# Performance work log

Measured on AMD Instinct MI355X. Metric: run time of the kernel, lower is better.

Reference implementation:

```python
import jax, jax.numpy as jnp
import numpy as np

EMB, HEADS, T_BLK = 1024, 16, 2048
B, T = 2, 2048
HD = EMB // HEADS


def setup_inputs() -> dict:
    key = jax.random.key(0)
    ks = jax.random.split(key, 9)
    s = 1.0 / np.sqrt(EMB)
    return {
        "x": jax.random.normal(ks[0], (B, T, EMB), jnp.float32),
        "Wq": jax.random.normal(ks[1], (EMB, EMB), jnp.float32) * s,
        "bq": jax.random.normal(ks[2], (EMB,), jnp.float32) * s,
        "Wk": jax.random.normal(ks[3], (EMB, EMB), jnp.float32) * s,
        "bk": jax.random.normal(ks[4], (EMB,), jnp.float32) * s,
        "Wv": jax.random.normal(ks[5], (EMB, EMB), jnp.float32) * s,
        "bv": jax.random.normal(ks[6], (EMB,), jnp.float32) * s,
        "Wo": jax.random.normal(ks[7], (EMB, EMB), jnp.float32) * s,
        "bo": jax.random.normal(ks[8], (EMB,), jnp.float32) * s,
    }


def reference(x, Wq, bq, Wk, bk, Wv, bv, Wo, bo):
    # eval mode: dropout is identity
    Bn, Tn, C = x.shape
    def proj(W, b):
        y = x @ W.T + b                      # [B,T,C]
        return y.reshape(Bn, Tn, HEADS, HD).transpose(0, 2, 1, 3)  # [B,H,T,hd]
    q, k, v = proj(Wq, bq), proj(Wk, bk), proj(Wv, bv)
    scores = jnp.einsum('bhqd,bhkd->bhqk', q, k) * (HD ** -0.5)  # [B,H,T,T]
    causal = jnp.tril(jnp.ones((Tn, Tn), dtype=bool))
    scores = jnp.where(causal, scores, -jnp.inf)
    w = jax.nn.softmax(scores, axis=-1)
    out = jnp.einsum('bhqk,bhkd->bhqd', w, v)                    # [B,H,T,hd]
    out = out.transpose(0, 2, 1, 3).reshape(Bn, Tn, C)
    return out @ Wo.T + bo
```

## Files before the change

### kernel.cpp

```cpp
#include <hip/hip_runtime.h>
#include <stdint.h>

#define EMB   1024
#define HEADS 16
#define HD    64
#define BB    2
#define TT    2048
#define MTOT  (BB*TT)
#define LDA   72
#define LDP   72

#define ELX (4194304u)
#define ELW (1048576u)

#define CSCALE (0.125f * 1.44269504088896f)

typedef __attribute__((ext_vector_type(8))) short short8;
typedef __attribute__((ext_vector_type(4))) float f32x4;
typedef __attribute__((ext_vector_type(4))) unsigned short us4;

__device__ __forceinline__ float bf2f(ushort u) {
  union { uint32_t u; float f; } x; x.u = ((uint32_t)u) << 16; return x.f;
}
__device__ __forceinline__ ushort f2bf(float f) {
  union { float f; uint32_t u; } x; x.f = f;
  uint32_t u = x.u;
  u += 0x7fffu + ((u >> 16) & 1u);
  return (ushort)(u >> 16);
}
__device__ __forceinline__ ushort f2bf_trunc(float f) {
  union { float f; uint32_t u; } x; x.f = f;
  return (ushort)(x.u >> 16);
}
__device__ __forceinline__ uint32_t pack2(uint32_t lo, uint32_t hi) {
  return (lo >> 16) | (hi & 0xFFFF0000u);
}
__device__ __forceinline__ short8 pack8(f32x4 a, f32x4 b) {
  union { f32x4 v; uint32_t u[4]; } A, B;
  A.v = a; B.v = b;
  union { uint32_t d[4]; short8 s; } R;
  R.d[0] = pack2(A.u[0], A.u[1]);
  R.d[1] = pack2(A.u[2], A.u[3]);
  R.d[2] = pack2(B.u[0], B.u[1]);
  R.d[3] = pack2(B.u[2], B.u[3]);
  return R.s;
}
__device__ __forceinline__ short8 cvt8_rne(const float* f) {
  f32x4 a = *(const f32x4*)f;
  f32x4 b = *(const f32x4*)(f + 4);
  short8 r;
  r[0] = (short)f2bf(a[0]); r[1] = (short)f2bf(a[1]);
  r[2] = (short)f2bf(a[2]); r[3] = (short)f2bf(a[3]);
  r[4] = (short)f2bf(b[0]); r[5] = (short)f2bf(b[1]);
  r[6] = (short)f2bf(b[2]); r[7] = (short)f2bf(b[3]);
  return r;
}

__global__ void detect_dtype(const uint32_t* __restrict__ x, int* __restrict__ flag) {
  const int lane = threadIdx.x & 63;
  int cnt = 0;
#pragma unroll
  for (int i = 0; i < 4; ++i) {
    const uint32_t v = x[lane * 4 + i];
    const uint32_t e = ((v & 0xFFFFu) >> 7) & 0xFFu;
    cnt += (e >= 0x70u && e <= 0x8Fu) ? 1 : 0;
  }
#pragma unroll
  for (int off = 1; off < 64; off <<= 1) cnt += __shfl_xor(cnt, off);
  if (lane == 0) *flag = (cnt > 128) ? 1 : 0;
}

__global__ __launch_bounds__(256) void convert3(const void* __restrict__ w0,
                                                const void* __restrict__ w1,
                                                const void* __restrict__ w2,
                                                ushort* __restrict__ dst,
                                                const int* __restrict__ flag) {
  const size_t i = ((size_t)blockIdx.x * 256 + threadIdx.x) * 8;
  const int wi = (int)(i >> 20);
  const size_t off = i & (ELW - 1);
  const void* src = (wi == 0) ? w0 : (wi == 1) ? w1 : w2;
  if (*flag) *(short8*)(dst + i) = *(const short8*)((const ushort*)src + off);
  else       *(short8*)(dst + i) = cvt8_rne((const float*)src + off);
}

template<bool ABF>
__device__ __forceinline__ void gemm_qkv64(const void* __restrict__ Ap,
                                           const ushort* __restrict__ Wp,
                                           int m0, int n0,
                                           ushort* As, ushort* Ws,
                                           f32x4 acc[4][2]) {
  const int tid  = threadIdx.x;
  const int w    = tid >> 6;
  const int lane = tid & 63;
  const int quad = lane >> 4;
  const int l16  = lane & 15;
  const int arow = tid >> 2;
  const int acol = (tid & 3) * 16;
  const int brow = tid >> 1;
  const int bcol = (tid & 1) * 32;

  const size_t aoff = (size_t)(m0 + arow) * EMB + acol;
  const size_t boff = (size_t)(n0 + brow) * EMB + bcol;

  short8 ab[3][2];
  f32x4  af[3][4];
  short8 wb[3][4];

#pragma unroll
  for (int s = 0; s < 2; ++s) {
    if constexpr (ABF) {
      ab[s][0] = *(const short8*)((const ushort*)Ap + aoff + 64 * s);
      ab[s][1] = *(const short8*)((const ushort*)Ap + aoff + 64 * s + 8);
    } else {
#pragma unroll
      for (int i = 0; i < 4; ++i)
        af[s][i] = *(const f32x4*)((const float*)Ap + aoff + 64 * s + 4 * i);
    }
#pragma unroll
    for (int i = 0; i < 4; ++i)
      wb[s][i] = *(const short8*)(Wp + boff + 64 * s + 8 * i);
  }

#pragma unroll
  for (int it = 0; it < 16; ++it) {
    const int k0 = it * 64;
    const int cur = it % 3, nxt = (it + 2) % 3;
    __syncthreads();
    if constexpr (ABF) {
      *(short8*)&As[arow * LDP + acol]     = ab[cur][0];
      *(short8*)&As[arow * LDP + acol + 8] = ab[cur][1];
    } else {
      *(short8*)&As[arow * LDP + acol]     = pack8(af[cur][0], af[cur][1]);
      *(short8*)&As[arow * LDP + acol + 8] = pack8(af[cur][2], af[cur][3]);
    }
#pragma unroll
    for (int i = 0; i < 4; ++i) *(short8*)&Ws[brow * LDP + bcol + 8 * i] = wb[cur][i];
    if (it + 2 < 16) {
      const int kn = k0 + 128;
      if constexpr (ABF) {
        ab[nxt][0] = *(const short8*)((const ushort*)Ap + aoff + kn);
        ab[nxt][1] = *(const short8*)((const ushort*)Ap + aoff + kn + 8);
      } else {
#pragma unroll
        for (int i = 0; i < 4; ++i)
          af[nxt][i] = *(const f32x4*)((const float*)Ap + aoff + kn + 4 * i);
      }
#pragma unroll
      for (int i = 0; i < 4; ++i)
        wb[nxt][i] = *(const short8*)(Wp + boff + kn + 8 * i);
    }
    __syncthreads();

#pragma unroll
    for (int ks = 0; ks < 2; ++ks) {
      short8 a_[4], b_[2];
#pragma unroll
      for (int i = 0; i < 4; ++i)
        a_[i] = *(const short8*)&As[(i * 16 + l16) * LDP + ks * 32 + quad * 8];
#pragma unroll
      for (int i = 0; i < 2; ++i)
        b_[i] = *(const short8*)&Ws[(w * 32 + i * 16 + l16) * LDP + ks * 32 + quad * 8];
#pragma unroll
      for (int mi = 0; mi < 4; ++mi)
#pragma unroll
        for (int ni = 0; ni < 2; ++ni)
          acc[mi][ni] = __builtin_amdgcn_mfma_f32_16x16x32_bf16(a_[mi], b_[ni], acc[mi][ni], 0, 0, 0);
    }
  }
}

__device__ __forceinline__ void qkv_epi64(f32x4 acc[4][2], int mt, int n0, int mat,
                                          const void* bias, int isbf,
                                          ushort* qo, ushort* ko, ushort* vo) {
  const int tid  = threadIdx.x;
  const int w    = tid >> 6;
  const int lane = tid & 63;
  const int quad = lane >> 4;
  const int l16  = lane & 15;
  ushort* dst = (mat == 0) ? qo : ko;
  const float sc = (mat == 0) ? CSCALE : 1.0f;

#pragma unroll
  for (int ni = 0; ni < 2; ++ni) {
    const int n = n0 + w * 32 + ni * 16 + l16;
    const float bv_ = isbf ? bf2f(((const ushort*)bias)[n]) : ((const float*)bias)[n];
    const int hh = n >> 6, d = n & 63;
#pragma unroll
    for (int mi = 0; mi < 4; ++mi) {
      const int mbase = mt * 64 + mi * 16 + quad * 4;
      const int b = mbase >> 11, t = mbase & (TT - 1);
      if (mat == 2) {
        us4 pk;
#pragma unroll
        for (int r = 0; r < 4; ++r) pk[r] = f2bf(acc[mi][ni][r] + bv_);
        *(us4*)&vo[((size_t)((b * HEADS + hh) * HD + d)) * TT + t] = pk;
      } else {
#pragma unroll
        for (int r = 0; r < 4; ++r)
          dst[((size_t)((b * HEADS + hh) * TT + t + r)) * HD + d] = f2bf((acc[mi][ni][r] + bv_) * sc);
      }
    }
  }
}

__global__ __launch_bounds__(256) void qkv_pipe(const void* __restrict__ x,
                                                const ushort* __restrict__ w3,
                                                const void* __restrict__ bq,
                                                const void* __restrict__ bk,
                                                const void* __restrict__ bv,
                                                ushort* __restrict__ qo,
                                                ushort* __restrict__ ko,
                                                ushort* __restrict__ vo,
                                                const int* __restrict__ flag) {
  __shared__ __align__(16) ushort As[64 * LDP];
  __shared__ __align__(16) ushort Ws[128 * LDP];
  const int xcd = blockIdx.x & 7;
  const int i   = blockIdx.x >> 3;
  const int nt  = xcd * 3 + (i % 3);
  const int mt  = i / 3;
  const int mat = nt >> 3;
  const int n0  = (nt & 7) * 128;
  const ushort* W  = w3 + (size_t)mat * ELW;
  const void* bias = (mat == 0) ? bq : (mat == 1) ? bk : bv;

  f32x4 acc[4][2];
#pragma unroll
  for (int a = 0; a < 4; ++a)
#pragma unroll
    for (int b = 0; b < 2; ++b) acc[a][b] = (f32x4){0.f, 0.f, 0.f, 0.f};

  const int isbf = *flag;
  if (isbf) gemm_qkv64<true >(x, W, mt * 64, n0, As, Ws, acc);
  else      gemm_qkv64<false>(x, W, mt * 64, n0, As, Ws, acc);
  qkv_epi64(acc, mt, n0, mat, bias, isbf, qo, ko, vo);
}

__global__ __launch_bounds__(256) void attn3(const ushort* __restrict__ qw,
                                             const ushort* __restrict__ kw,
                                             const ushort* __restrict__ vtw,
                                             ushort* __restrict__ out) {
  __shared__ __align__(16) ushort Ks[64 * LDA];
  __shared__ __align__(16) ushort Vts[64 * LDA];
  __shared__ __align__(16) ushort Ps[4][16 * LDA];

  const int bid = blockIdx.x;
  const int j  = bid >> 8;
  const int r8 = bid & 255;
  const int qh = r8 & 31;
  const int bh = j * 8 + (r8 >> 5);
  int qt;
  if      (j == 0) qt = qh;
  else if (j == 1) qt = 31 - qh;
  else if (j == 2) qt = (qh + 16) & 31;
  else             qt = 31 - ((qh + 16) & 31);
  const int h = bh & (HEADS - 1);
  const int b = bh >> 4;

  const int tid  = threadIdx.x;
  const int w    = tid >> 6;
  const int lane = tid & 63;
  const int quad = lane >> 4;
  const int l16  = lane & 15;

  const size_t hoff = ((size_t)(b * HEADS + h)) * TT * HD;
  const ushort* Qg = qw + hoff;
  const ushort* Kg = kw + hoff;
  const ushort* Vg = vtw + hoff;
  const int q0 = qt * 64;

  short8 qf[2];
  {
    const ushort* qrow = Qg + (size_t)(q0 + w * 16 + l16) * HD;
    qf[0] = *(const short8*)(qrow + quad * 8);
    qf[1] = *(const short8*)(qrow + 32 + quad * 8);
  }

  const int row = tid >> 2;
  const int c0  = (tid & 3) * 16;
  const ushort* Kbase = Kg + (size_t)row * HD + c0;
  const ushort* Vbase = Vg + (size_t)row * TT + c0;

  float ls[4] = {0.f, 0.f, 0.f, 0.f};
  f32x4 O[4];
#pragma unroll
  for (int ni = 0; ni < 4; ++ni) O[ni] = (f32x4){0.f, 0.f, 0.f, 0.f};

  auto compute_tile = [&](int kt) {
    f32x4 s[4];
#pragma unroll
    for (int ni = 0; ni < 4; ++ni) s[ni] = (f32x4){0.f, 0.f, 0.f, 0.f};
#pragma unroll
    for (int ks = 0; ks < 2; ++ks) {
#pragma unroll
      for (int ni = 0; ni < 4; ++ni) {
        short8 kb = *(const short8*)&Ks[(ni * 16 + l16) * LDA + ks * 32 + quad * 8];
        s[ni] = __builtin_amdgcn_mfma_f32_16x16x32_bf16(qf[ks], kb, s[ni], 0, 0, 0);
      }
    }
    if (kt == qt) {
#pragma unroll
      for (int ni = 0; ni < 4; ++ni) {
        const int kk = ni * 16 + l16;
#pragma unroll
        for (int r = 0; r < 4; ++r)
          if (kk > w * 16 + quad * 4 + r) s[ni][r] = -__builtin_inff();
      }
    }
#pragma unroll
    for (int ni = 0; ni < 4; ++ni)
#pragma unroll
      for (int r = 0; r < 4; ++r) {
        const float p = exp2f(s[ni][r]);
        s[ni][r] = p;
        ls[r] += p;
      }
#pragma unroll
    for (int ni = 0; ni < 4; ++ni)
#pragma unroll
      for (int r = 0; r < 4; ++r)
        Ps[w][(quad * 4 + r) * LDA + ni * 16 + l16] = f2bf_trunc(s[ni][r]);
#pragma unroll
    for (int ks = 0; ks < 2; ++ks) {
      short8 a = *(const short8*)&Ps[w][l16 * LDA + ks * 32 + quad * 8];
#pragma unroll
      for (int ni = 0; ni < 4; ++ni) {
        short8 vb = *(const short8*)&Vts[(ni * 16 + l16) * LDA + ks * 32 + quad * 8];
        O[ni] = __builtin_amdgcn_mfma_f32_16x16x32_bf16(a, vb, O[ni], 0, 0, 0);
      }
    }
  };

  short8 ak0, ak1, av0, av1;
  short8 bk0, bk1, bv0, bv1;

  ak0 = *(const short8*)(Kbase);
  ak1 = *(const short8*)(Kbase + 8);
  av0 = *(const short8*)(Vbase);
  av1 = *(const short8*)(Vbase + 8);

  for (int kt = 0; kt <= qt; ) {
    __syncthreads();
    *(short8*)&Ks[row * LDA + c0]      = ak0;
    *(short8*)&Ks[row * LDA + c0 + 8]  = ak1;
    *(short8*)&Vts[row * LDA + c0]     = av0;
    *(short8*)&Vts[row * LDA + c0 + 8] = av1;
    if (kt + 1 <= qt) {
      const size_t ko_ = (size_t)(kt + 1) * 64 * HD;
      bk0 = *(const short8*)(Kbase + ko_);
      bk1 = *(const short8*)(Kbase + ko_ + 8);
      bv0 = *(const short8*)(Vbase + (kt + 1) * 64);
      bv1 = *(const short8*)(Vbase + (kt + 1) * 64 + 8);
    }
    __syncthreads();
    compute_tile(kt);
    ++kt;
    if (kt > qt) break;

    __syncthreads();
    *(short8*)&Ks[row * LDA + c0]      = bk0;
    *(short8*)&Ks[row * LDA + c0 + 8]  = bk1;
    *(short8*)&Vts[row * LDA + c0]     = bv0;
    *(short8*)&Vts[row * LDA + c0 + 8] = bv1;
    if (kt + 1 <= qt) {
      const size_t ko_ = (size_t)(kt + 1) * 64 * HD;
      ak0 = *(const short8*)(Kbase + ko_);
      ak1 = *(const short8*)(Kbase + ko_ + 8);
      av0 = *(const short8*)(Vbase + (kt + 1) * 64);
      av1 = *(const short8*)(Vbase + (kt + 1) * 64 + 8);
    }
    __syncthreads();
    compute_tile(kt);
    ++kt;
  }

#pragma unroll
  for (int r = 0; r < 4; ++r) {
#pragma unroll
    for (int off = 1; off < 16; off <<= 1) ls[r] += __shfl_xor(ls[r], off);
    const float inv = 1.0f / ls[r];
    const int t = q0 + w * 16 + quad * 4 + r;
#pragma unroll
    for (int ni = 0; ni < 4; ++ni) {
      out[((size_t)(b * TT + t)) * EMB + h * HD + ni * 16 + l16] = f2bf(O[ni][r] * inv);
    }
  }
}

template<bool WBF>
__device__ __forceinline__ void proj_core(const ushort* __restrict__ A,
                                          const void* __restrict__ Wo,
                                          int m0, int n0,
                                          ushort* As, ushort* Ws,
                                          f32x4 acc[4][2]) {
  const int tid  = threadIdx.x;
  const int w    = tid >> 6;
  const int lane = tid & 63;
  const int quad = lane >> 4;
  const int l16  = lane & 15;
  const int arow = tid >> 2;
  const int acol = (tid & 3) * 16;
  const int brow = tid >> 1;
  const int bcol = (tid & 1) * 32;

  const size_t aoff = (size_t)(m0 + arow) * EMB + acol;
  const size_t boff = (size_t)(n0 + brow) * EMB + bcol;

  short8 ab[3][2];
  short8 wb[3][4];
  f32x4  wf[3][8];

#pragma unroll
  for (int s = 0; s < 2; ++s) {
    ab[s][0] = *(const short8*)(A + aoff + 64 * s);
    ab[s][1] = *(const short8*)(A + aoff + 64 * s + 8);
    if constexpr (WBF) {
#pragma unroll
      for (int i = 0; i < 4; ++i)
        wb[s][i] = *(const short8*)((const ushort*)Wo + boff + 64 * s + 8 * i);
    } else {
#pragma unroll
      for (int i = 0; i < 8; ++i)
        wf[s][i] = *(const f32x4*)((const float*)Wo + boff + 64 * s + 4 * i);
    }
  }

#pragma unroll
  for (int it = 0; it < 16; ++it) {
    const int k0 = it * 64;
    const int cur = it % 3, nxt = (it + 2) % 3;
    __syncthreads();
    *(short8*)&As[arow * LDP + acol]     = ab[cur][0];
    *(short8*)&As[arow * LDP + acol + 8] = ab[cur][1];
    if constexpr (WBF) {
#pragma unroll
      for (int i = 0; i < 4; ++i) *(short8*)&Ws[brow * LDP + bcol + 8 * i] = wb[cur][i];
    } else {
#pragma unroll
      for (int i = 0; i < 4; ++i)
        *(short8*)&Ws[brow * LDP + bcol + 8 * i] = pack8(wf[cur][2 * i], wf[cur][2 * i + 1]);
    }
    if (it + 2 < 16) {
      const int kn = k0 + 128;
      ab[nxt][0] = *(const short8*)(A + aoff + kn);
      ab[nxt][1] = *(const short8*)(A + aoff + kn + 8);
      if constexpr (WBF) {
#pragma unroll
        for (int i = 0; i < 4; ++i)
          wb[nxt][i] = *(const short8*)((const ushort*)Wo + boff + kn + 8 * i);
      } else {
#pragma unroll
        for (int i = 0; i < 8; ++i)
          wf[nxt][i] = *(const f32x4*)((const float*)Wo + boff + kn + 4 * i);
      }
    }
    __syncthreads();

#pragma unroll
    for (int ks = 0; ks < 2; ++ks) {
      short8 a_[4], b_[2];
#pragma unroll
      for (int i = 0; i < 4; ++i)
        a_[i] = *(const short8*)&As[(i * 16 + l16) * LDP + ks * 32 + quad * 8];
#pragma unroll
      for (int i = 0; i < 2; ++i)
        b_[i] = *(const short8*)&Ws[(w * 32 + i * 16 + l16) * LDP + ks * 32 + quad * 8];
#pragma unroll
      for (int mi = 0; mi < 4; ++mi)
#pragma unroll
        for (int ni = 0; ni < 2; ++ni)
          acc[mi][ni] = __builtin_amdgcn_mfma_f32_16x16x32_bf16(a_[mi], b_[ni], acc[mi][ni], 0, 0, 0);
    }
  }
}

__global__ __launch_bounds__(256) void proj_pipe(const ushort* __restrict__ A,
                                                 const void* __restrict__ Wo,
                                                 const void* __restrict__ bo,
                                                 void* __restrict__ out,
                                                 const int* __restrict__ flag) {
  __shared__ __align__(16) ushort As[64 * LDP];
  __shared__ __align__(16) ushort Ws[128 * LDP];
  const int nt = blockIdx.x & 7;
  const int mt = blockIdx.x >> 3;
  const int n0 = nt * 128;
  const int m0 = mt * 64;

  f32x4 acc[4][2];
#pragma unroll
  for (int i = 0; i < 4; ++i)
#pragma unroll
    for (int jj = 0; jj < 2; ++jj) acc[i][jj] = (f32x4){0.f, 0.f, 0.f, 0.f};

  const int isbf = *flag;
  if (isbf) proj_core<true >(A, Wo, m0, n0, As, Ws, acc);
  else      proj_core<false>(A, Wo, m0, n0, As, Ws, acc);

  const int tid  = threadIdx.x;
  const int w    = tid >> 6;
  const int lane = tid & 63;
  const int quad = lane >> 4;
  const int l16  = lane & 15;

#pragma unroll
  for (int ni = 0; ni < 2; ++ni) {
    const int n = n0 + w * 32 + ni * 16 + l16;
    const float bv_ = isbf ? bf2f(((const ushort*)bo)[n]) : ((const float*)bo)[n];
#pragma unroll
    for (int mi = 0; mi < 4; ++mi) {
#pragma unroll
      for (int r = 0; r < 4; ++r) {
        const int m = m0 + mi * 16 + quad * 4 + r;
        const float v = acc[mi][ni][r] + bv_;
        if (isbf) ((ushort*)out)[(size_t)m * EMB + n] = f2bf(v);
        else      ((float*) out)[(size_t)m * EMB + n] = v;
      }
    }
  }
}

extern "C" void kernel_launch(void* const* d_in, const int* in_sizes, int n_in,
                              void* d_out, int out_size, void* d_ws, size_t ws_size,
                              hipStream_t stream) {
  const void* x  = d_in[0];
  const void* Wq = d_in[1];
  const void* bq = d_in[2];
  const void* Wk = d_in[3];
  const void* bk = d_in[4];
  const void* Wv = d_in[5];
  const void* bv = d_in[6];
  const void* Wo = d_in[7];
  const void* bo = d_in[8];

  int* flag = (int*)d_ws;
  ushort* base = (ushort*)((char*)d_ws + 256);

  ushort* q_ws  = base;
  ushort* k_ws  = q_ws + ELX;
  ushort* vt_ws = k_ws + ELX;
  ushort* w3    = vt_ws + ELX;
  ushort* o_ws  = vt_ws + ELX;

  detect_dtype<<<dim3(1), dim3(64), 0, stream>>>((const uint32_t*)x, flag);
  convert3<<<dim3(1536), dim3(256), 0, stream>>>(Wq, Wk, Wv, w3, flag);
  qkv_pipe<<<dim3(1536), dim3(256), 0, stream>>>(x, w3, bq, bk, bv,
                                                 q_ws, k_ws, vt_ws, flag);
  attn3<<<dim3(1024), dim3(256), 0, stream>>>(q_ws, k_ws, vt_ws, o_ws);
  proj_pipe<<<dim3(512), dim3(256), 0, stream>>>(o_ws, Wo, bo, d_out, flag);
}
```

Measured before the change: 232.7 us.

## Transpose QK^T MFMA for packed P stores and retile output projection to 128x64

The attention kernel now swaps the MFMA operands for QK^T so each lane holds four consecutive key columns of one query row. The probabilities can then be packed two per dword and written to shared memory as a single 8-byte store instead of 16 scalar stores. The row-sum reduction becomes a per-lane partial sum followed by a cross-quad shuffle. The output projection switches from 64x128 to 128x64 tiles, with each wave owning 32 rows and all 64 columns, which changes global load vectorisation and the A/W reuse balance.

Measured after the change: 218.3 us. -6.2%, faster.

```diff
diff --git a/kernel.cpp b/kernel.cpp
--- a/kernel.cpp
+++ b/kernel.cpp
@@ -27,10 +27,6 @@
   uint32_t u = x.u;
   u += 0x7fffu + ((u >> 16) & 1u);
   return (ushort)(u >> 16);
-}
-__device__ __forceinline__ ushort f2bf_trunc(float f) {
-  union { float f; uint32_t u; } x; x.f = f;
-  return (ushort)(x.u >> 16);
 }
 __device__ __forceinline__ uint32_t pack2(uint32_t lo, uint32_t hi) {
   return (lo >> 16) | (hi & 0xFFFF0000u);
@@ -280,7 +276,7 @@
   const ushort* Kbase = Kg + (size_t)row * HD + c0;
   const ushort* Vbase = Vg + (size_t)row * TT + c0;
 
-  float ls[4] = {0.f, 0.f, 0.f, 0.f};
+  float lsp[4] = {0.f, 0.f, 0.f, 0.f};
   f32x4 O[4];
 #pragma unroll
   for (int ni = 0; ni < 4; ++ni) O[ni] = (f32x4){0.f, 0.f, 0.f, 0.f};
@@ -294,31 +290,29 @@
 #pragma unroll
       for (int ni = 0; ni < 4; ++ni) {
         short8 kb = *(const short8*)&Ks[(ni * 16 + l16) * LDA + ks * 32 + quad * 8];
-        s[ni] = __builtin_amdgcn_mfma_f32_16x16x32_bf16(qf[ks], kb, s[ni], 0, 0, 0);
+        s[ni] = __builtin_amdgcn_mfma_f32_16x16x32_bf16(kb, qf[ks], s[ni], 0, 0, 0);
       }
     }
     if (kt == qt) {
+      const int qq = w * 16 + l16;
 #pragma unroll
       for (int ni = 0; ni < 4; ++ni) {
-        const int kk = ni * 16 + l16;
 #pragma unroll
         for (int r = 0; r < 4; ++r)
-          if (kk > w * 16 + quad * 4 + r) s[ni][r] = -__builtin_inff();
-      }
-    }
-#pragma unroll
-    for (int ni = 0; ni < 4; ++ni)
-#pragma unroll
-      for (int r = 0; r < 4; ++r) {
-        const float p = exp2f(s[ni][r]);
-        s[ni][r] = p;
-        ls[r] += p;
-      }
-#pragma unroll
-    for (int ni = 0; ni < 4; ++ni)
-#pragma unroll
-      for (int r = 0; r < 4; ++r)
-        Ps[w][(quad * 4 + r) * LDA + ni * 16 + l16] = f2bf_trunc(s[ni][r]);
+          if (ni * 16 + quad * 4 + r > qq) s[ni][r] = -__builtin_inff();
+      }
+    }
+#pragma unroll
+    for (int ni = 0; ni < 4; ++ni) {
+      union { float f; uint32_t u; } p0, p1, p2, p3;
+      p0.f = exp2f(s[ni][0]); p1.f = exp2f(s[ni][1]);
+      p2.f = exp2f(s[ni][2]); p3.f = exp2f(s[ni][3]);
+      lsp[ni] += (p0.f + p1.f) + (p2.f + p3.f);
+      uint2 dw;
+      dw.x = pack2(p0.u, p1.u);
+      dw.y = pack2(p2.u, p3.u);
+      *(uint2*)&Ps[w][l16 * LDA + ni * 16 + quad * 4] = dw;
+    }
 #pragma unroll
     for (int ks = 0; ks < 2; ++ks) {
       short8 a = *(const short8*)&Ps[w][l16 * LDA + ks * 32 + quad * 8];
@@ -332,7 +326,6 @@
 
   short8 ak0, ak1, av0, av1;
   short8 bk0, bk1, bv0, bv1;
-
   ak0 = *(const short8*)(Kbase);
   ak1 = *(const short8*)(Kbase + 8);
   av0 = *(const short8*)(Vbase);
@@ -373,11 +366,13 @@
     ++kt;
   }
 
+  float lst = (lsp[0] + lsp[1]) + (lsp[2] + lsp[3]);
+  lst += __shfl_xor(lst, 16);
+  lst += __shfl_xor(lst, 32);
+
 #pragma unroll
   for (int r = 0; r < 4; ++r) {
-#pragma unroll
-    for (int off = 1; off < 16; off <<= 1) ls[r] += __shfl_xor(ls[r], off);
-    const float inv = 1.0f / ls[r];
+    const float inv = 1.0f / __shfl(lst, (lane & 48) | (quad * 4 + r));
     const int t = q0 + w * 16 + quad * 4 + r;
 #pragma unroll
     for (int ni = 0; ni < 4; ++ni) {
@@ -391,35 +386,35 @@
                                           const void* __restrict__ Wo,
                                           int m0, int n0,
                                           ushort* As, ushort* Ws,
-                                          f32x4 acc[4][2]) {
+                                          f32x4 acc[2][4]) {
   const int tid  = threadIdx.x;
   const int w    = tid >> 6;
   const int lane = tid & 63;
   const int quad = lane >> 4;
   const int l16  = lane & 15;
-  const int arow = tid >> 2;
-  const int acol = (tid & 3) * 16;
-  const int brow = tid >> 1;
-  const int bcol = (tid & 1) * 32;
+  const int arow = tid >> 1;
+  const int acol = (tid & 1) * 32;
+  const int brow = tid >> 2;
+  const int bcol = (tid & 3) * 16;
 
   const size_t aoff = (size_t)(m0 + arow) * EMB + acol;
   const size_t boff = (size_t)(n0 + brow) * EMB + bcol;
 
-  short8 ab[3][2];
-  short8 wb[3][4];
-  f32x4  wf[3][8];
+  short8 ab[3][4];
+  short8 wb[3][2];
+  f32x4  wf[3][4];
 
 #pragma unroll
   for (int s = 0; s < 2; ++s) {
-    ab[s][0] = *(const short8*)(A + aoff + 64 * s);
-    ab[s][1] = *(const short8*)(A + aoff + 64 * s + 8);
+#pragma unroll
+    for (int i = 0; i < 4; ++i)
+      ab[s][i] = *(const short8*)(A + aoff + 64 * s + 8 * i);
     if constexpr (WBF) {
+      wb[s][0] = *(const short8*)((const ushort*)Wo + boff + 64 * s);
+      wb[s][1] = *(const short8*)((const ushort*)Wo + boff + 64 * s + 8);
+    } else {
 #pragma unroll
       for (int i = 0; i < 4; ++i)
-        wb[s][i] = *(const short8*)((const ushort*)Wo + boff + 64 * s + 8 * i);
-    } else {
-#pragma unroll
-      for (int i = 0; i < 8; ++i)
         wf[s][i] = *(const f32x4*)((const float*)Wo + boff + 64 * s + 4 * i);
     }
   }
@@ -429,27 +424,27 @@
     const int k0 = it * 64;
     const int cur = it % 3, nxt = (it + 2) % 3;
     __syncthreads();
-    *(short8*)&As[arow * LDP + acol]     = ab[cur][0];
-    *(short8*)&As[arow * LDP + acol + 8] = ab[cur][1];
+#pragma unroll
+    for (int i = 0; i < 4; ++i)
+      *(short8*)&As[arow * LDP + acol + 8 * i] = ab[cur][i];
     if constexpr (WBF) {
-#pragma unroll
-      for (int i = 0; i < 4; ++i) *(short8*)&Ws[brow * LDP + bcol + 8 * i] = wb[cur][i];
+      *(short8*)&Ws[brow * LDP + bcol]     = wb[cur][0];
+      *(short8*)&Ws[brow * LDP + bcol + 8] = wb[cur][1];
     } else {
-#pragma unroll
-      for (int i = 0; i < 4; ++i)
-        *(short8*)&Ws[brow * LDP + bcol + 8 * i] = pack8(wf[cur][2 * i], wf[cur][2 * i + 1]);
+      *(short8*)&Ws[brow * LDP + bcol]     = pack8(wf[cur][0], wf[cur][1]);
+      *(short8*)&Ws[brow * LDP + bcol + 8] = pack8(wf[cur][2], wf[cur][3]);
     }
     if (it + 2 < 16) {
       const int kn = k0 + 128;
-      ab[nxt][0] = *(const short8*)(A + aoff + kn);
-      ab[nxt][1] = *(const short8*)(A + aoff + kn + 8);
+#pragma unroll
+      for (int i = 0; i < 4; ++i)
+        ab[nxt][i] = *(const short8*)(A + aoff + kn + 8 * i);
       if constexpr (WBF) {
+        wb[nxt][0] = *(const short8*)((const ushort*)Wo + boff + kn);
+        wb[nxt][1] = *(const short8*)((const ushort*)Wo + boff + kn + 8);
+      } else {
 #pragma unroll
         for (int i = 0; i < 4; ++i)
-          wb[nxt][i] = *(const short8*)((const ushort*)Wo + boff + kn + 8 * i);
-      } else {
-#pragma unroll
-        for (int i = 0; i < 8; ++i)
           wf[nxt][i] = *(const f32x4*)((const float*)Wo + boff + kn + 4 * i);
       }
     }
@@ -457,17 +452,17 @@
 
 #pragma unroll
     for (int ks = 0; ks < 2; ++ks) {
-      short8 a_[4], b_[2];
+      short8 a_[2], b_[4];
+#pragma unroll
+      for (int i = 0; i < 2; ++i)
+        a_[i] = *(const short8*)&As[(w * 32 + i * 16 + l16) * LDP + ks * 32 + quad * 8];
 #pragma unroll
       for (int i = 0; i < 4; ++i)
-        a_[i] = *(const short8*)&As[(i * 16 + l16) * LDP + ks * 32 + quad * 8];
-#pragma unroll
-      for (int i = 0; i < 2; ++i)
-        b_[i] = *(const short8*)&Ws[(w * 32 + i * 16 + l16) * LDP + ks * 32 + quad * 8];
-#pragma unroll
-      for (int mi = 0; mi < 4; ++mi)
-#pragma unroll
-        for (int ni = 0; ni < 2; ++ni)
+        b_[i] = *(const short8*)&Ws[(i * 16 + l16) * LDP + ks * 32 + quad * 8];
+#pragma unroll
+      for (int mi = 0; mi < 2; ++mi)
+#pragma unroll
+        for (int ni = 0; ni < 4; ++ni)
           acc[mi][ni] = __builtin_amdgcn_mfma_f32_16x16x32_bf16(a_[mi], b_[ni], acc[mi][ni], 0, 0, 0);
     }
   }
@@ -478,18 +473,18 @@
                                                  const void* __restrict__ bo,
                                                  void* __restrict__ out,
                                                  const int* __restrict__ flag) {
-  __shared__ __align__(16) ushort As[64 * LDP];
-  __shared__ __align__(16) ushort Ws[128 * LDP];
-  const int nt = blockIdx.x & 7;
-  const int mt = blockIdx.x >> 3;
-  const int n0 = nt * 128;
-  const int m0 = mt * 64;
-
-  f32x4 acc[4][2];
-#pragma unroll
-  for (int i = 0; i < 4; ++i)
-#pragma unroll
-    for (int jj = 0; jj < 2; ++jj) acc[i][jj] = (f32x4){0.f, 0.f, 0.f, 0.f};
+  __shared__ __align__(16) ushort As[128 * LDP];
+  __shared__ __align__(16) ushort Ws[64 * LDP];
+  const int nt = blockIdx.x & 15;
+  const int mt = blockIdx.x >> 4;
+  const int n0 = nt * 64;
+  const int m0 = mt * 128;
+
+  f32x4 acc[2][4];
+#pragma unroll
+  for (int i = 0; i < 2; ++i)
+#pragma unroll
+    for (int jj = 0; jj < 4; ++jj) acc[i][jj] = (f32x4){0.f, 0.f, 0.f, 0.f};
 
   const int isbf = *flag;
   if (isbf) proj_core<true >(A, Wo, m0, n0, As, Ws, acc);
@@ -502,14 +497,14 @@
   const int l16  = lane & 15;
 
 #pragma unroll
-  for (int ni = 0; ni < 2; ++ni) {
-    const int n = n0 + w * 32 + ni * 16 + l16;
+  for (int ni = 0; ni < 4; ++ni) {
+    const int n = n0 + ni * 16 + l16;
     const float bv_ = isbf ? bf2f(((const ushort*)bo)[n]) : ((const float*)bo)[n];
 #pragma unroll
-    for (int mi = 0; mi < 4; ++mi) {
+    for (int mi = 0; mi < 2; ++mi) {
 #pragma unroll
       for (int r = 0; r < 4; ++r) {
-        const int m = m0 + mi * 16 + quad * 4 + r;
+        const int m = m0 + w * 32 + mi * 16 + quad * 4 + r;
         const float v = acc[mi][ni][r] + bv_;
         if (isbf) ((ushort*)out)[(size_t)m * EMB + n] = f2bf(v);
         else      ((float*) out)[(size_t)m * EMB + n] = v;
```
